# Optimization experiments

Measured on AMD Instinct MI355X. Metric: run time of the kernel, lower is better.

Reference implementation:

```python
import jax, jax.numpy as jnp
import numpy as np

NUM_CP = 5
DEGREE = 4
GRID_LO, GRID_HI = -1.0, 1.0
G = 3  # grid points, set via set_grid_points(3)


def _precompute_basis():
    # knots = linspace(lo - degree*0.1, hi + degree*0.1, num_cp + degree + 1)
    knots = np.linspace(GRID_LO - DEGREE * 0.1, GRID_HI + DEGREE * 0.1, NUM_CP + DEGREE + 1)
    grid_points = np.linspace(GRID_LO, GRID_HI, G)
    basis = np.zeros((G, NUM_CP), dtype=np.float32)
    for i in range(NUM_CP):
        center = (knots[i + DEGREE // 2] + knots[i + DEGREE // 2 + 1]) / 2.0
        width = (knots[i + DEGREE + 1] - knots[i]) / 2.0
        basis[:, i] = np.exp(-((grid_points - center) / width) ** 2)
    basis_sum = basis.sum(axis=1, keepdims=True)
    return (basis / (basis_sum + 1e-6)).astype(np.float32)


def setup_inputs() -> dict:
    key = jax.random.key(0)
    k1, k2, k3, k4 = jax.random.split(key, 4)
    x = jax.random.normal(k1, (8, 2048, 2048), dtype=jnp.float32)
    control_points = jax.random.normal(k2, (NUM_CP,), dtype=jnp.float32) * 0.1
    base_weight = jax.random.normal(k3, (1,), dtype=jnp.float32)
    spline_weight = jax.random.normal(k4, (1,), dtype=jnp.float32)
    basis_values = jnp.asarray(_precompute_basis())
    return {"x": x, "control_points": control_points, "base_weight": base_weight,
            "spline_weight": spline_weight, "basis_values": basis_values}


def reference(x, control_points, base_weight, spline_weight, basis_values):
    x_clipped = jnp.clip(x, GRID_LO, GRID_HI)
    norm_x = (x_clipped - GRID_LO) / (GRID_HI - GRID_LO)
    grid_idx = norm_x * (G - 1)
    idx_low = jnp.clip(jnp.floor(grid_idx).astype(jnp.int32), 0, G - 1)
    idx_high = jnp.clip(jnp.ceil(grid_idx).astype(jnp.int32), 0, G - 1)
    frac = grid_idx - idx_low.astype(grid_idx.dtype)
    basis_low = basis_values[idx_low]    # [..., NUM_CP]
    basis_high = basis_values[idx_high]  # [..., NUM_CP]
    basis = basis_low * (1.0 - frac[..., None]) + basis_high * frac[..., None]
    y_spline = jnp.einsum('...c,c->...', basis, control_points)
    base = x * jax.nn.sigmoid(x)  # SiLU base_func
    return base_weight * base + spline_weight * y_spline
```

## Files before the change

### kernel.cpp

```cpp
#include <hip/hip_runtime.h>
#include <math.h>


__global__ __launch_bounds__(256) void bspline_act_v4(
    const float4* __restrict__ x4,
    const float*  __restrict__ cp,
    const float*  __restrict__ bw_p,
    const float*  __restrict__ sw_p,
    const float*  __restrict__ bv,
    float4*       __restrict__ out4,
    int n4)
{
    int i = blockIdx.x * blockDim.x + threadIdx.x;
    if (i >= n4) return;

    const float c0 = cp[0], c1 = cp[1], c2 = cp[2], c3 = cp[3], c4 = cp[4];
    const float s0 = bv[0]*c0  + bv[1]*c1  + bv[2]*c2  + bv[3]*c3  + bv[4]*c4;
    const float s1 = bv[5]*c0  + bv[6]*c1  + bv[7]*c2  + bv[8]*c3  + bv[9]*c4;
    const float s2 = bv[10]*c0 + bv[11]*c1 + bv[12]*c2 + bv[13]*c3 + bv[14]*c4;
    const float d0 = s1 - s0, d1 = s2 - s1;
    const float bw = bw_p[0], sw = sw_p[0];

    float4 v = x4[i];
    float xs[4] = {v.x, v.y, v.z, v.w};
    float r[4];
#pragma unroll
    for (int k = 0; k < 4; ++k) {
        float x  = xs[k];
        float t  = fminf(fmaxf(x, -1.0f), 1.0f) + 1.0f;
        float fl = floorf(t);
        float fr = t - fl;
        int   il = (int)fl;
        float sl = (il == 0) ? s0 : ((il == 1) ? s1 : s2);
        float dl = (il == 0) ? d0 : d1;
        float y  = sl + fr * dl;
        float sig = 1.0f / (1.0f + __expf(-x));
        r[k] = bw * (x * sig) + sw * y;
    }
    out4[i] = make_float4(r[0], r[1], r[2], r[3]);
}

__global__ void bspline_act_tail(
    const float* __restrict__ x,
    const float* __restrict__ cp,
    const float* __restrict__ bw_p,
    const float* __restrict__ sw_p,
    const float* __restrict__ bv,
    float*       __restrict__ out,
    int start, int n)
{
    int i = start + blockIdx.x * blockDim.x + threadIdx.x;
    if (i >= n) return;
    const float c0 = cp[0], c1 = cp[1], c2 = cp[2], c3 = cp[3], c4 = cp[4];
    const float s0 = bv[0]*c0  + bv[1]*c1  + bv[2]*c2  + bv[3]*c3  + bv[4]*c4;
    const float s1 = bv[5]*c0  + bv[6]*c1  + bv[7]*c2  + bv[8]*c3  + bv[9]*c4;
    const float s2 = bv[10]*c0 + bv[11]*c1 + bv[12]*c2 + bv[13]*c3 + bv[14]*c4;
    const float d0 = s1 - s0, d1 = s2 - s1;
    const float bw = bw_p[0], sw = sw_p[0];

    float xv = x[i];
    float t  = fminf(fmaxf(xv, -1.0f), 1.0f) + 1.0f;
    float fl = floorf(t);
    float fr = t - fl;
    int   il = (int)fl;
    float sl = (il == 0) ? s0 : ((il == 1) ? s1 : s2);
    float dl = (il == 0) ? d0 : d1;
    float y  = sl + fr * dl;
    float sig = 1.0f / (1.0f + __expf(-xv));
    out[i] = bw * (xv * sig) + sw * y;
}

extern "C" void kernel_launch(void* const* d_in, const int* in_sizes, int n_in,
                              void* d_out, int out_size, void* d_ws, size_t ws_size,
                              hipStream_t stream) {
    const float* x  = (const float*)d_in[0];
    const float* cp = (const float*)d_in[1];
    const float* bw = (const float*)d_in[2];
    const float* sw = (const float*)d_in[3];
    const float* bv = (const float*)d_in[4];
    float* out = (float*)d_out;

    const int n  = in_sizes[0];
    const int n4 = n / 4;
    const int rem_start = n4 * 4;

    if (n4 > 0) {
        const int block = 256;
        const int grid  = (n4 + block - 1) / block;
        bspline_act_v4<<<grid, block, 0, stream>>>(
            (const float4*)x, cp, bw, sw, bv, (float4*)out, n4);
    }
    if (rem_start < n) {
        const int rem = n - rem_start;
        bspline_act_tail<<<(rem + 255) / 256, 256, 0, stream>>>(
            x, cp, bw, sw, bv, out, rem_start, n);
    }
}
```

Measured before the change: 226.6 us.

## Process four float4 per thread with nontemporal loads and simplified spline math

Each thread now loads four strided float4 vectors with nontemporal loads up front, then computes them and writes them back with nontemporal stores. The piecewise-linear spline is rewritten as two clamped FMAs with sw folded into the constants, which removes the floor/select logic. The sigmoid reciprocal uses the hardware rcp builtin. This aims to improve memory-level parallelism and bypass cache pollution on a bandwidth-bound elementwise kernel, at some cost in reciprocal precision.

```diff
diff --git a/kernel.cpp b/kernel.cpp
--- a/kernel.cpp
+++ b/kernel.cpp
@@ -2,42 +2,72 @@
 #include <math.h>
 
 
-__global__ __launch_bounds__(256) void bspline_act_v4(
-    const float4* __restrict__ x4,
-    const float*  __restrict__ cp,
-    const float*  __restrict__ bw_p,
-    const float*  __restrict__ sw_p,
-    const float*  __restrict__ bv,
-    float4*       __restrict__ out4,
+typedef float f32x4 __attribute__((ext_vector_type(4)));
+
+#define TPB 256
+#define VPT 4
+
+__device__ __forceinline__ float fast_rcp(float a) {
+#if defined(__has_builtin)
+#if __has_builtin(__builtin_amdgcn_rcpf)
+    return __builtin_amdgcn_rcpf(a);
+#else
+    return 1.0f / a;
+#endif
+#else
+    return 1.0f / a;
+#endif
+}
+
+__global__ __launch_bounds__(TPB) void bspline_act_v5(
+    const f32x4* __restrict__ x4,
+    const float* __restrict__ cp,
+    const float* __restrict__ bw_p,
+    const float* __restrict__ sw_p,
+    const float* __restrict__ bv,
+    f32x4*       __restrict__ out4,
     int n4)
 {
-    int i = blockIdx.x * blockDim.x + threadIdx.x;
-    if (i >= n4) return;
-
     const float c0 = cp[0], c1 = cp[1], c2 = cp[2], c3 = cp[3], c4 = cp[4];
     const float s0 = bv[0]*c0  + bv[1]*c1  + bv[2]*c2  + bv[3]*c3  + bv[4]*c4;
     const float s1 = bv[5]*c0  + bv[6]*c1  + bv[7]*c2  + bv[8]*c3  + bv[9]*c4;
     const float s2 = bv[10]*c0 + bv[11]*c1 + bv[12]*c2 + bv[13]*c3 + bv[14]*c4;
-    const float d0 = s1 - s0, d1 = s2 - s1;
     const float bw = bw_p[0], sw = sw_p[0];
+    const float S1 = sw * s1;
+    const float D0 = sw * (s1 - s0);
+    const float D1 = sw * (s2 - s1);
 
-    float4 v = x4[i];
-    float xs[4] = {v.x, v.y, v.z, v.w};
-    float r[4];
+    const int base = blockIdx.x * (TPB * VPT) + threadIdx.x;
+
+    f32x4 v[VPT];
 #pragma unroll
-    for (int k = 0; k < 4; ++k) {
-        float x  = xs[k];
-        float t  = fminf(fmaxf(x, -1.0f), 1.0f) + 1.0f;
-        float fl = floorf(t);
-        float fr = t - fl;
-        int   il = (int)fl;
-        float sl = (il == 0) ? s0 : ((il == 1) ? s1 : s2);
-        float dl = (il == 0) ? d0 : d1;
-        float y  = sl + fr * dl;
-        float sig = 1.0f / (1.0f + __expf(-x));
-        r[k] = bw * (x * sig) + sw * y;
+    for (int k = 0; k < VPT; ++k) {
+        const int idx = base + k * TPB;
+        if (idx < n4) {
+            v[k] = __builtin_nontemporal_load(&x4[idx]);
+        } else {
+            f32x4 z = {0.f, 0.f, 0.f, 0.f};
+            v[k] = z;
+        }
     }
-    out4[i] = make_float4(r[0], r[1], r[2], r[3]);
+
+#pragma unroll
+    for (int k = 0; k < VPT; ++k) {
+        const int idx = base + k * TPB;
+        f32x4 xv = v[k];
+        f32x4 r;
+#pragma unroll
+        for (int e = 0; e < 4; ++e) {
+            float x  = xv[e];
+            float u  = fminf(fmaxf(x, -1.0f), 1.0f);
+            float ys = fmaf(D0, fminf(u, 0.0f),
+                       fmaf(D1, fmaxf(u, 0.0f), S1));
+            float ex  = __expf(-x);
+            float sig = fast_rcp(1.0f + ex);
+            r[e] = fmaf(bw * x, sig, ys);
+        }
+        if (idx < n4) __builtin_nontemporal_store(r, &out4[idx]);
+    }
 }
 
 __global__ void bspline_act_tail(
@@ -55,19 +85,17 @@
     const float s0 = bv[0]*c0  + bv[1]*c1  + bv[2]*c2  + bv[3]*c3  + bv[4]*c4;
     const float s1 = bv[5]*c0  + bv[6]*c1  + bv[7]*c2  + bv[8]*c3  + bv[9]*c4;
     const float s2 = bv[10]*c0 + bv[11]*c1 + bv[12]*c2 + bv[13]*c3 + bv[14]*c4;
-    const float d0 = s1 - s0, d1 = s2 - s1;
     const float bw = bw_p[0], sw = sw_p[0];
+    const float S1 = sw * s1;
+    const float D0 = sw * (s1 - s0);
+    const float D1 = sw * (s2 - s1);
 
     float xv = x[i];
-    float t  = fminf(fmaxf(xv, -1.0f), 1.0f) + 1.0f;
-    float fl = floorf(t);
-    float fr = t - fl;
-    int   il = (int)fl;
-    float sl = (il == 0) ? s0 : ((il == 1) ? s1 : s2);
-    float dl = (il == 0) ? d0 : d1;
-    float y  = sl + fr * dl;
-    float sig = 1.0f / (1.0f + __expf(-xv));
-    out[i] = bw * (xv * sig) + sw * y;
+    float u  = fminf(fmaxf(xv, -1.0f), 1.0f);
+    float ys = fmaf(D0, fminf(u, 0.0f), fmaf(D1, fmaxf(u, 0.0f), S1));
+    float ex  = __expf(-xv);
+    float sig = fast_rcp(1.0f + ex);
+    out[i] = fmaf(bw * xv, sig, ys);
 }
 
 extern "C" void kernel_launch(void* const* d_in, const int* in_sizes, int n_in,
@@ -85,10 +113,10 @@
     const int rem_start = n4 * 4;
 
     if (n4 > 0) {
-        const int block = 256;
-        const int grid  = (n4 + block - 1) / block;
-        bspline_act_v4<<<grid, block, 0, stream>>>(
-            (const float4*)x, cp, bw, sw, bv, (float4*)out, n4);
+        const int per_block = TPB * VPT;
+        const int grid = (n4 + per_block - 1) / per_block;
+        bspline_act_v5<<<grid, TPB, 0, stream>>>(
+            (const f32x4*)x, cp, bw, sw, bv, (f32x4*)out, n4);
     }
     if (rem_start < n) {
         const int rem = n - rem_start;
```

Result: no change. 226.0 us (-0.3%).
